# Kernel tuning notes

Measured on AMD Instinct MI355X. Metric: run time of the kernel, lower is better.

Reference implementation:

```python
import jax, jax.numpy as jnp
import numpy as np

B, H, W, C = 8, 256, 256, 180
HEADS, HEAD_DIM = 6, 30
WIN = (16, 16)
SPARSITY = 4


def setup_inputs() -> dict:
    key = jax.random.key(0)
    ks = jax.random.split(key, 6)
    bg = 1.0 / np.sqrt(3 * HEAD_DIM)          # ExpertGather init bound (1/sqrt(head_dim_out)) approx
    bs = 1.0 / np.sqrt(C * HEADS)             # ExpertScatter init bound
    return {
        "x": jax.random.normal(ks[0], (B, H, W, C), jnp.float32),
        "Wr": jax.random.normal(ks[1], (HEADS, C), jnp.float32) / np.sqrt(C),      # router Linear(dim, heads, bias=False)
        "Wqkv": jax.random.uniform(ks[2], (HEADS, C, 3 * HEAD_DIM), jnp.float32, -bg, bg),
        "Wo": jax.random.uniform(ks[3], (HEADS, HEAD_DIM, C), jnp.float32, -bs, bs),
        "Wp": jax.random.normal(ks[4], (C, C), jnp.float32) / np.sqrt(C),          # proj Linear(dim, dim)
        "bp": jnp.zeros((C,), jnp.float32),
    }


def reference(x, Wr, Wqkv, Wo, Wp, bp):
    wh, ww = WIN
    L = wh * ww  # tokens per window = 256
    # ---- window_partition: (B,H,W,C) -> (Bw, L, C)
    xw = x.reshape(B, H // wh, wh, W // ww, ww, C).transpose(0, 1, 3, 2, 4, 5).reshape(-1, L, C)
    Bw = xw.shape[0]
    # ---- router: sigmoid(Linear) -> (Bw, L, heads)
    logits = jax.nn.sigmoid(jnp.einsum('blc,ec->ble', xw, Wr))
    k = min(max(L // SPARSITY, 2), L)  # static: 64
    # ---- top-k including first token (get_topk_includefirst)
    tail = logits[:, 1:, :].transpose(0, 2, 1)          # (Bw, heads, L-1)
    tv, ti = jax.lax.top_k(tail, k - 1)                 # top k-1 over tokens 1..L-1
    ti = ti + 1
    fv = logits[:, 0, :][:, :, None]                    # (Bw, heads, 1)
    fi = jnp.zeros((Bw, HEADS, 1), jnp.int32)
    vals = jnp.concatenate([fv, tv], axis=2)            # (Bw, heads, k) sigmoid gates
    idx = jnp.concatenate([fi, ti], axis=2)             # (Bw, heads, k) token indices
    idx_flat = idx.reshape(Bw, HEADS * k)
    # ---- ExpertGather: per-head gather then per-head linear -> QKV
    Xg = jnp.take_along_axis(xw, idx_flat[:, :, None], axis=1).reshape(Bw, HEADS, k, C)
    qkv = jnp.einsum('beki,eij->bekj', Xg, Wqkv)        # (Bw, heads, k, 3*head_dim)
    Q, K, V = jnp.split(qkv, 3, axis=-1)
    # ---- scaled dot product attention over the k routed tokens per head
    scores = jnp.einsum('bekd,bejd->bekj', Q, K) / np.sqrt(HEAD_DIM).astype(np.float32)
    attn = jnp.einsum('bekj,bejd->bekd', jax.nn.softmax(scores, axis=-1), V)
    attn = attn * vals[..., None]                       # sigmoid gating
    # ---- ExpertScatter: per-head linear then scatter-add combine
    pre = jnp.einsum('bekj,eji->beki', attn, Wo)        # (Bw, heads, k, C)
    scattered = jnp.zeros((Bw, L, C), x.dtype).at[
        jnp.arange(Bw)[:, None], idx_flat
    ].add(pre.reshape(Bw, HEADS * k, C))
    # ---- window_reverse: (Bw, L, C) -> (B, H, W, C)
    y = scattered.reshape(B, H // wh, W // ww, wh, ww, C).transpose(0, 1, 3, 2, 4, 5).reshape(B, H, W, C)
    # ---- output projection (dropout prob = 0)
    return jnp.einsum('bhwc,oc->bhwo', y, Wp) + bp
```

## Files before the change

kernel.cpp:

```cpp
#include <hip/hip_runtime.h>
#include <math.h>

#define NB 8
#define NH 256
#define NW 256
#define NC 180
#define NE 6
#define HD 30
#define NL 256
#define NK 64
#define NWIN 2048

typedef __attribute__((ext_vector_type(8))) short bf16x8;
typedef __attribute__((ext_vector_type(4))) float f32x4;

union FU { bf16x8 f; unsigned u[4]; unsigned short s[8]; };

static __device__ __forceinline__ unsigned short f2bf(float x) {
    unsigned u = __float_as_uint(x);
    unsigned r = (u + 0x7FFFu + ((u >> 16) & 1u)) >> 16;
    return (unsigned short)r;
}
static __device__ __forceinline__ unsigned pk2(float a, float b) {
    return (unsigned)f2bf(a) | ((unsigned)f2bf(b) << 16);
}
static __device__ __forceinline__ bf16x8 ld8(const unsigned short* p) {
    FU t;
    *(uint2*)&t.u[0] = *(const uint2*)p;
    *(uint2*)&t.u[2] = *(const uint2*)(p + 16);
    return t.f;
}
static __device__ __forceinline__ bf16x8 ld16(const unsigned short* p) {
    FU t;
    *(uint4*)&t.u[0] = *(const uint4*)p;
    return t.f;
}
static __device__ __forceinline__ bf16x8 ld8q(const unsigned short* p) {
    FU t;
    t.u[0] = *(const unsigned*)p;
    t.u[1] = *(const unsigned*)(p + 2);
    t.u[2] = *(const unsigned*)(p + 16);
    t.u[3] = *(const unsigned*)(p + 18);
    return t.f;
}
static __device__ __forceinline__ bf16x8 pack8(float4 a, float4 b) {
    FU t;
    t.u[0] = pk2(a.x, a.y); t.u[1] = pk2(a.z, a.w);
    t.u[2] = pk2(b.x, b.y); t.u[3] = pk2(b.z, b.w);
    return t.f;
}

__global__ __launch_bounds__(256) void k_prep(
    const float* __restrict__ Wqkv, const float* __restrict__ Wo,
    const float* __restrict__ Wp,
    unsigned short* __restrict__ Wqkv_t, unsigned short* __restrict__ Wcomb_t)
{
    int i = blockIdx.x * 256 + threadIdx.x;
    if (i < NE * 96 * 192) {
        int q = i / 192, rem = i % 192;
        int h = q / 96, np = q % 96;
        int kt = rem / 32, lg = (rem % 32) / 8, e = rem % 8;
        int k = 32 * kt + 4 * lg + (e < 4 ? e : 12 + e);
        int sec = np >> 5, r = np & 31;
        float v = (r < 30 && k < NC) ? Wqkv[((long)h * NC + k) * 90 + sec * 30 + r] : 0.f;
        Wqkv_t[i] = f2bf(v);
    }
    if (i < NE * 192 * 32) {
        int q = i / 32, rem = i % 32;
        int h = q / 192, o = q % 192;
        int lg = rem / 8, e = rem % 8;
        int d = 4 * lg + (e < 4 ? e : 12 + e);
        float acc = 0.f;
        if (o < NC && d < HD) {
            const float* wo = Wo + ((long)h * HD + d) * NC;
            const float* wp = Wp + (long)o * NC;
            for (int c = 0; c < NC; ++c) acc += wo[c] * wp[c];
        }
        Wcomb_t[i] = f2bf(acc);
    }
}

__global__ __launch_bounds__(256) void k_router_topk(
    const float* __restrict__ x, const float* __restrict__ Wr,
    int* __restrict__ idx_g, float* __restrict__ vals_g)
{
    __shared__ float wr_s[NE * NC];
    __shared__ __align__(16) float xs[32 * 181];
    __shared__ float lg[NE * NL];

    const int w   = blockIdx.x;
    const int tid = threadIdx.x;
    const int b = w >> 8, hb = (w >> 4) & 15, wb = w & 15;
    const long win_base = (((long)b * NH + hb * 16) * NW + wb * 16) * NC;

    for (int f = tid; f < NE * NC; f += 256) wr_s[f] = Wr[f];
    __syncthreads();

    for (int tile = 0; tile < 8; ++tile) {
        for (int f = tid; f < 32 * NC; f += 256) {
            int tl = f / NC, ch = f % NC;
            int tok = tile * 32 + tl;
            int r = tok >> 4, cl = tok & 15;
            xs[tl * 181 + ch] = x[win_base + ((long)r * NW + cl) * NC + ch];
        }
        __syncthreads();
        if (tid < 192) {
            int tl = tid & 31, e = tid >> 5;
            float acc = 0.f;
            for (int c = 0; c < NC; ++c) acc += xs[tl * 181 + c] * wr_s[e * NC + c];
            lg[e * NL + tile * 32 + tl] = 1.0f / (1.0f + expf(-acc));
        }
        __syncthreads();
    }

    unsigned long long* keys = (unsigned long long*)xs;
    #pragma unroll
    for (int e = 0; e < NE; ++e) {
        unsigned kb = __float_as_uint(lg[e * NL + tid]);
        unsigned long long comp =
            ((unsigned long long)kb << 32) | (unsigned)(0xFFFFFFFFu - tid);
        if (tid == 0) comp = 0ull;
        keys[e * NL + tid] = comp;
    }
    __syncthreads();

    for (int k = 2; k <= 256; k <<= 1) {
        for (int j = k >> 1; j > 0; j >>= 1) {
            const int i = tid, ixj = i ^ j;
            if (ixj > i) {
                const bool up = ((i & k) == 0);
                #pragma unroll
                for (int e = 0; e < NE; ++e) {
                    unsigned long long a  = keys[e * NL + i];
                    unsigned long long bv = keys[e * NL + ixj];
                    bool sw = up ? (a < bv) : (a > bv);
                    if (sw) { keys[e * NL + i] = bv; keys[e * NL + ixj] = a; }
                }
            }
            __syncthreads();
        }
    }

    if (tid < NK - 1) {
        #pragma unroll
        for (int e = 0; e < NE; ++e) {
            unsigned long long kk = keys[e * NL + tid];
            int t = (int)(0xFFFFFFFFu - (unsigned)kk);
            idx_g[(w * NE + e) * NK + 1 + tid]  = t;
            vals_g[(w * NE + e) * NK + 1 + tid] = __uint_as_float((unsigned)(kk >> 32));
        }
    }
    if (tid == 0) {
        #pragma unroll
        for (int e = 0; e < NE; ++e) {
            idx_g[(w * NE + e) * NK]  = 0;
            vals_g[(w * NE + e) * NK] = lg[e * NL];
        }
    }
}

__global__ __launch_bounds__(256, 3) void k_attn(
    const float* __restrict__ x,
    const unsigned short* __restrict__ Wqkv_t,
    const int* __restrict__ idx_g, const float* __restrict__ vals_g,
    unsigned short* __restrict__ at_g)
{
    __shared__ char sm[34816];
    const int tid = threadIdx.x;
    const int wv = tid >> 6;
    const int ln = tid & 63;
    const int lr = ln & 15;
    const int lg = ln >> 4;

    const int bid = (blockIdx.x & 7) * 384 + (blockIdx.x >> 3);
    const int id = bid * 4 + wv;
    const int w = id / 6;
    const int h = id % 6;
    const int b = w >> 8, hb = (w >> 4) & 15, wb = w & 15;
    const long win_base = (((long)b * NH + hb * 16) * NW + wb * 16) * NC;

    unsigned short* q_s = (unsigned short*)(sm + wv * 8704);
    unsigned short* k_s = q_s + 2176;

    int tokr[4];
    #pragma unroll
    for (int t = 0; t < 4; ++t)
        tokr[t] = idx_g[((long)w * NE + h) * NK + 16 * t + lr];

    f32x4 acc[6][4];
    #pragma unroll
    for (int nt = 0; nt < 6; ++nt)
        #pragma unroll
        for (int mt = 0; mt < 4; ++mt) acc[nt][mt] = (f32x4){0.f, 0.f, 0.f, 0.f};

    const unsigned short* bb = Wqkv_t + ((long)h * 96 + lr) * 192 + 8 * lg;
    #pragma unroll
    for (int kt = 0; kt < 6; ++kt) {
        bf16x8 Amt[4];
        #pragma unroll
        for (int mt = 0; mt < 4; ++mt) {
            const float* xr = x + win_base +
                ((long)(tokr[mt] >> 4) * NW + (tokr[mt] & 15)) * NC;
            if (kt < 5) {
                float4 a  = *(const float4*)(xr + 4 * lg + 32 * kt);
                float4 b2 = *(const float4*)(xr + 4 * lg + 32 * kt + 16);
                Amt[mt] = pack8(a, b2);
            } else {
                float4 a  = *(const float4*)(xr + 4 * lg + 160);
                float4 b2 = make_float4(0.f, 0.f, 0.f, 0.f);
                if (lg == 0) b2 = *(const float4*)(xr + 176);
                Amt[mt] = pack8(a, b2);
            }
        }
        #pragma unroll
        for (int nt = 0; nt < 6; ++nt) {
            bf16x8 B = ld16(bb + nt * (16 * 192) + kt * 32);
            #pragma unroll
            for (int mt = 0; mt < 4; ++mt)
                acc[nt][mt] = __builtin_amdgcn_mfma_f32_16x16x32_bf16(Amt[mt], B, acc[nt][mt], 0, 0, 0);
        }
    }

    #pragma unroll
    for (int nt = 0; nt < 4; ++nt) {
        unsigned short* dst = (nt < 2 ? q_s : k_s) + 16 * (nt & 1) + lr;
        #pragma unroll
        for (int mt = 0; mt < 4; ++mt) {
            int row = 16 * mt + 4 * lg;
            dst[(row + 0) * 34] = f2bf(acc[nt][mt][0]);
            dst[(row + 1) * 34] = f2bf(acc[nt][mt][1]);
            dst[(row + 2) * 34] = f2bf(acc[nt][mt][2]);
            dst[(row + 3) * 34] = f2bf(acc[nt][mt][3]);
        }
    }
    unsigned V32[4][2][2];
    #pragma unroll
    for (int j = 0; j < 2; ++j)
        #pragma unroll
        for (int mt = 0; mt < 4; ++mt) {
            V32[mt][j][0] = pk2(acc[4 + j][mt][0], acc[4 + j][mt][1]);
            V32[mt][j][1] = pk2(acc[4 + j][mt][2], acc[4 + j][mt][3]);
        }

    __syncthreads();

    f32x4 s[4][4];
    {
        bf16x8 Bq[4];
        #pragma unroll
        for (int nt = 0; nt < 4; ++nt)
            Bq[nt] = ld8q(q_s + (16 * nt + lr) * 34 + 4 * lg);
        #pragma unroll
        for (int amt = 0; amt < 4; ++amt) {
            bf16x8 Ak = ld8q(k_s + (16 * amt + lr) * 34 + 4 * lg);
            #pragma unroll
            for (int nt = 0; nt < 4; ++nt)
                s[amt][nt] = __builtin_amdgcn_mfma_f32_16x16x32_bf16(
                    Ak, Bq[nt], (f32x4){0.f, 0.f, 0.f, 0.f}, 0, 0, 0);
        }
    }

    float gsc[4];
    #pragma unroll
    for (int nt = 0; nt < 4; ++nt) {
        float mx = -1e30f;
        #pragma unroll
        for (int amt = 0; amt < 4; ++amt)
            #pragma unroll
            for (int r = 0; r < 4; ++r) mx = fmaxf(mx, s[amt][nt][r]);
        mx = fmaxf(mx, __shfl_xor(mx, 16));
        mx = fmaxf(mx, __shfl_xor(mx, 32));
        float sum = 0.f;
        #pragma unroll
        for (int amt = 0; amt < 4; ++amt)
            #pragma unroll
            for (int r = 0; r < 4; ++r) {
                float p = __expf((s[amt][nt][r] - mx) * 0.18257418583505536f);
                s[amt][nt][r] = p;
                sum += p;
            }
        sum += __shfl_xor(sum, 16);
        sum += __shfl_xor(sum, 32);
        gsc[nt] = vals_g[((long)w * NE + h) * NK + 16 * nt + lr] / sum;
    }

    bf16x8 Av[2][2];
    #pragma unroll
    for (int amt = 0; amt < 2; ++amt)
        #pragma unroll
        for (int kt = 0; kt < 2; ++kt) {
            FU t;
            t.u[0] = V32[2 * kt][amt][0];
            t.u[1] = V32[2 * kt][amt][1];
            t.u[2] = V32[2 * kt + 1][amt][0];
            t.u[3] = V32[2 * kt + 1][amt][1];
            Av[amt][kt] = t.f;
        }
    #pragma unroll
    for (int nt = 0; nt < 4; ++nt) {
        bf16x8 Pb[2];
        float g = gsc[nt];
        #pragma unroll
        for (int kt = 0; kt < 2; ++kt) {
            FU t;
            t.u[0] = pk2(s[2 * kt][nt][0] * g, s[2 * kt][nt][1] * g);
            t.u[1] = pk2(s[2 * kt][nt][2] * g, s[2 * kt][nt][3] * g);
            t.u[2] = pk2(s[2 * kt + 1][nt][0] * g, s[2 * kt + 1][nt][1] * g);
            t.u[3] = pk2(s[2 * kt + 1][nt][2] * g, s[2 * kt + 1][nt][3] * g);
            Pb[kt] = t.f;
        }
        f32x4 a0 = (f32x4){0.f, 0.f, 0.f, 0.f};
        a0 = __builtin_amdgcn_mfma_f32_16x16x32_bf16(Av[0][0], Pb[0], a0, 0, 0, 0);
        a0 = __builtin_amdgcn_mfma_f32_16x16x32_bf16(Av[0][1], Pb[1], a0, 0, 0, 0);
        f32x4 a1 = (f32x4){0.f, 0.f, 0.f, 0.f};
        a1 = __builtin_amdgcn_mfma_f32_16x16x32_bf16(Av[1][0], Pb[0], a1, 0, 0, 0);
        a1 = __builtin_amdgcn_mfma_f32_16x16x32_bf16(Av[1][1], Pb[1], a1, 0, 0, 0);
        unsigned short* row = at_g + (((long)h * NWIN + w) * 64 + 16 * nt + lr) * 32 + 8 * lg;
        *(uint4*)row = make_uint4(pk2(a0[0], a0[1]), pk2(a0[2], a0[3]),
                                  pk2(a1[0], a1[1]), pk2(a1[2], a1[3]));
    }
}

__global__ __launch_bounds__(384, 2) void k_scatter(
    const unsigned short* __restrict__ at_g,
    const unsigned short* __restrict__ Wcomb_t,
    const float* __restrict__ bp,
    const int* __restrict__ idx_g,
    float* __restrict__ out)
{
    __shared__ float outf[256 * 49];
    __shared__ unsigned char idx_s[NE * NK];

    const int w = blockIdx.x;
    const int tid = threadIdx.x;
    const int b = w >> 8, hb = (w >> 4) & 15, wb = w & 15;

    const int wv = tid >> 6;
    const int ln = tid & 63;
    const int lr = ln & 15;
    const int lg = ln >> 4;

    idx_s[tid] = (unsigned char)idx_g[(long)w * NE * NK + tid];

    const int wcol = wv % 3;
    const int nth  = wv / 3;

    bf16x8 Bt[NE][2];
    #pragma unroll
    for (int h = 0; h < NE; ++h)
        #pragma unroll
        for (int t = 0; t < 2; ++t) {
            const int nt = 2 * nth + t;
            Bt[h][t] = ld16(at_g + (((long)h * NWIN + w) * 64 + 16 * nt + lr) * 32 + 8 * lg);
        }
    __syncthreads();

    int tokk[NE][2];
    #pragma unroll
    for (int h = 0; h < NE; ++h)
        #pragma unroll
        for (int t = 0; t < 2; ++t)
            tokk[h][t] = idx_s[h * NK + 16 * (2 * nth + t) + lr];

    #pragma unroll
    for (int p = 0; p < 4; ++p) {
        for (int f = tid; f < 256 * 49; f += 384) outf[f] = 0.f;
        __syncthreads();

        #pragma unroll
        for (int h = 0; h < NE; ++h) {
            bf16x8 Aw = ld16(Wcomb_t + ((long)h * 192 + p * 48 + 16 * wcol + lr) * 32 + 8 * lg);
            #pragma unroll
            for (int t = 0; t < 2; ++t) {
                f32x4 acc = __builtin_amdgcn_mfma_f32_16x16x32_bf16(
                    Aw, Bt[h][t], (f32x4){0.f, 0.f, 0.f, 0.f}, 0, 0, 0);
                float* dst = outf + tokk[h][t] * 49 + 16 * wcol + 4 * lg;
                dst[0] += acc[0];
                dst[1] += acc[1];
                dst[2] += acc[2];
                dst[3] += acc[3];
            }
            __syncthreads();
        }

        const int nf4 = (p == 3) ? 9 : 12;
        for (int f = tid; f < 256 * nf4; f += 384) {
            int t = f / nf4, j = f % nf4;
            int c = 48 * p + 4 * j;
            float4 o;
            o.x = outf[t * 49 + 4 * j]     + bp[c];
            o.y = outf[t * 49 + 4 * j + 1] + bp[c + 1];
            o.z = outf[t * 49 + 4 * j + 2] + bp[c + 2];
            o.w = outf[t * 49 + 4 * j + 3] + bp[c + 3];
            long obase = (((long)b * NH + hb * 16 + (t >> 4)) * NW + wb * 16 + (t & 15)) * NC + c;
            *(float4*)(out + obase) = o;
        }
        __syncthreads();
    }
}

extern "C" void kernel_launch(void* const* d_in, const int* in_sizes, int n_in,
                              void* d_out, int out_size, void* d_ws, size_t ws_size,
                              hipStream_t stream) {
    const float* x    = (const float*)d_in[0];
    const float* Wr   = (const float*)d_in[1];
    const float* Wqkv = (const float*)d_in[2];
    const float* Wo   = (const float*)d_in[3];
    const float* Wp   = (const float*)d_in[4];
    const float* bp   = (const float*)d_in[5];
    float* out = (float*)d_out;

    char* ws = (char*)d_ws;
    unsigned short* Wqkv_t  = (unsigned short*)ws;
    unsigned short* Wcomb_t = (unsigned short*)(ws + 221184);
    int*   idx_g  = (int*)(ws + 294912);
    float* vals_g = (float*)(ws + 294912 + (size_t)NWIN * NE * NK * 4);
    unsigned short* at_g = (unsigned short*)(ws + 294912 + 2 * (size_t)NWIN * NE * NK * 4);

    k_prep<<<432, 256, 0, stream>>>(Wqkv, Wo, Wp, Wqkv_t, Wcomb_t);
    k_router_topk<<<NWIN, 256, 0, stream>>>(x, Wr, idx_g, vals_g);
    k_attn<<<3072, 256, 0, stream>>>(x, Wqkv_t, idx_g, vals_g, at_g);
    k_scatter<<<NWIN, 384, 0, stream>>>(at_g, Wcomb_t, bp, idx_g, out);
}
```

Before: 569.4 us.

## Fuse attention and scatter kernels into one per-window block with LDS handoff

Merges k_attn and k_scatter into a single kernel in which each 384-thread block handles one window and each of its six waves computes one head. The attention output now stays in shared memory instead of going through a global bf16 buffer, and the routing indices are staged once in LDS. This removes a kernel launch and a global write/read round trip of the attention output. The cost is a larger shared-memory footprint per block (about 77 KB), which may reduce occupancy. The scatter phase also loses the register prefetch of its B operands and has to wait for all heads to finish first.

```diff
diff --git a/kernel.cpp b/kernel.cpp
--- a/kernel.cpp
+++ b/kernel.cpp
@@ -23,12 +23,6 @@
 }
 static __device__ __forceinline__ unsigned pk2(float a, float b) {
     return (unsigned)f2bf(a) | ((unsigned)f2bf(b) << 16);
-}
-static __device__ __forceinline__ bf16x8 ld8(const unsigned short* p) {
-    FU t;
-    *(uint2*)&t.u[0] = *(const uint2*)p;
-    *(uint2*)&t.u[2] = *(const uint2*)(p + 16);
-    return t.f;
 }
 static __device__ __forceinline__ bf16x8 ld16(const unsigned short* p) {
     FU t;
@@ -159,33 +153,39 @@
     }
 }
 
-__global__ __launch_bounds__(256, 3) void k_attn(
+__global__ __launch_bounds__(384, 3) void k_fused(
     const float* __restrict__ x,
     const unsigned short* __restrict__ Wqkv_t,
+    const unsigned short* __restrict__ Wcomb_t,
+    const float* __restrict__ bp,
     const int* __restrict__ idx_g, const float* __restrict__ vals_g,
-    unsigned short* __restrict__ at_g)
+    float* __restrict__ out)
 {
-    __shared__ char sm[34816];
+    __shared__ char smA[52224];
+    __shared__ unsigned short at_s[NE * 64 * 32];
+    __shared__ unsigned char idx_s[NE * NK];
+
+    const int w = blockIdx.x;
     const int tid = threadIdx.x;
+    const int b = w >> 8, hb = (w >> 4) & 15, wb = w & 15;
+    const long win_base = (((long)b * NH + hb * 16) * NW + wb * 16) * NC;
+
     const int wv = tid >> 6;
     const int ln = tid & 63;
     const int lr = ln & 15;
     const int lg = ln >> 4;
-
-    const int bid = (blockIdx.x & 7) * 384 + (blockIdx.x >> 3);
-    const int id = bid * 4 + wv;
-    const int w = id / 6;
-    const int h = id % 6;
-    const int b = w >> 8, hb = (w >> 4) & 15, wb = w & 15;
-    const long win_base = (((long)b * NH + hb * 16) * NW + wb * 16) * NC;
-
-    unsigned short* q_s = (unsigned short*)(sm + wv * 8704);
+    const int h = wv;
+
+    idx_s[tid] = (unsigned char)idx_g[(long)w * NE * NK + tid];
+    __syncthreads();
+
+    unsigned short* q_s = (unsigned short*)(smA + h * 8704);
     unsigned short* k_s = q_s + 2176;
 
     int tokr[4];
     #pragma unroll
     for (int t = 0; t < 4; ++t)
-        tokr[t] = idx_g[((long)w * NE + h) * NK + 16 * t + lr];
+        tokr[t] = idx_s[h * NK + 16 * t + lr];
 
     f32x4 acc[6][4];
     #pragma unroll
@@ -315,52 +315,15 @@
         f32x4 a1 = (f32x4){0.f, 0.f, 0.f, 0.f};
         a1 = __builtin_amdgcn_mfma_f32_16x16x32_bf16(Av[1][0], Pb[0], a1, 0, 0, 0);
         a1 = __builtin_amdgcn_mfma_f32_16x16x32_bf16(Av[1][1], Pb[1], a1, 0, 0, 0);
-        unsigned short* row = at_g + (((long)h * NWIN + w) * 64 + 16 * nt + lr) * 32 + 8 * lg;
+        unsigned short* row = at_s + ((h * 64 + 16 * nt + lr) * 32 + 8 * lg);
         *(uint4*)row = make_uint4(pk2(a0[0], a0[1]), pk2(a0[2], a0[3]),
                                   pk2(a1[0], a1[1]), pk2(a1[2], a1[3]));
     }
-}
-
-__global__ __launch_bounds__(384, 2) void k_scatter(
-    const unsigned short* __restrict__ at_g,
-    const unsigned short* __restrict__ Wcomb_t,
-    const float* __restrict__ bp,
-    const int* __restrict__ idx_g,
-    float* __restrict__ out)
-{
-    __shared__ float outf[256 * 49];
-    __shared__ unsigned char idx_s[NE * NK];
-
-    const int w = blockIdx.x;
-    const int tid = threadIdx.x;
-    const int b = w >> 8, hb = (w >> 4) & 15, wb = w & 15;
-
-    const int wv = tid >> 6;
-    const int ln = tid & 63;
-    const int lr = ln & 15;
-    const int lg = ln >> 4;
-
-    idx_s[tid] = (unsigned char)idx_g[(long)w * NE * NK + tid];
-
+    __syncthreads();
+
+    float* outf = (float*)smA;
     const int wcol = wv % 3;
     const int nth  = wv / 3;
-
-    bf16x8 Bt[NE][2];
-    #pragma unroll
-    for (int h = 0; h < NE; ++h)
-        #pragma unroll
-        for (int t = 0; t < 2; ++t) {
-            const int nt = 2 * nth + t;
-            Bt[h][t] = ld16(at_g + (((long)h * NWIN + w) * 64 + 16 * nt + lr) * 32 + 8 * lg);
-        }
-    __syncthreads();
-
-    int tokk[NE][2];
-    #pragma unroll
-    for (int h = 0; h < NE; ++h)
-        #pragma unroll
-        for (int t = 0; t < 2; ++t)
-            tokk[h][t] = idx_s[h * NK + 16 * (2 * nth + t) + lr];
 
     #pragma unroll
     for (int p = 0; p < 4; ++p) {
@@ -368,17 +331,20 @@
         __syncthreads();
 
         #pragma unroll
-        for (int h = 0; h < NE; ++h) {
-            bf16x8 Aw = ld16(Wcomb_t + ((long)h * 192 + p * 48 + 16 * wcol + lr) * 32 + 8 * lg);
+        for (int hh = 0; hh < NE; ++hh) {
+            bf16x8 Aw = ld16(Wcomb_t + ((long)hh * 192 + p * 48 + 16 * wcol + lr) * 32 + 8 * lg);
             #pragma unroll
             for (int t = 0; t < 2; ++t) {
-                f32x4 acc = __builtin_amdgcn_mfma_f32_16x16x32_bf16(
-                    Aw, Bt[h][t], (f32x4){0.f, 0.f, 0.f, 0.f}, 0, 0, 0);
-                float* dst = outf + tokk[h][t] * 49 + 16 * wcol + 4 * lg;
-                dst[0] += acc[0];
-                dst[1] += acc[1];
-                dst[2] += acc[2];
-                dst[3] += acc[3];
+                const int nt = 2 * nth + t;
+                bf16x8 Bt = ld16(at_s + ((hh * 64 + 16 * nt + lr) * 32 + 8 * lg));
+                f32x4 pacc = __builtin_amdgcn_mfma_f32_16x16x32_bf16(
+                    Aw, Bt, (f32x4){0.f, 0.f, 0.f, 0.f}, 0, 0, 0);
+                int tok = idx_s[hh * NK + 16 * nt + lr];
+                float* dst = outf + tok * 49 + 16 * wcol + 4 * lg;
+                dst[0] += pacc[0];
+                dst[1] += pacc[1];
+                dst[2] += pacc[2];
+                dst[3] += pacc[3];
             }
             __syncthreads();
         }
@@ -415,10 +381,9 @@
     unsigned short* Wcomb_t = (unsigned short*)(ws + 221184);
     int*   idx_g  = (int*)(ws + 294912);
     float* vals_g = (float*)(ws + 294912 + (size_t)NWIN * NE * NK * 4);
-    unsigned short* at_g = (unsigned short*)(ws + 294912 + 2 * (size_t)NWIN * NE * NK * 4);
 
     k_prep<<<432, 256, 0, stream>>>(Wqkv, Wo, Wp, Wqkv_t, Wcomb_t);
     k_router_topk<<<NWIN, 256, 0, stream>>>(x, Wr, idx_g, vals_g);
-    k_attn<<<3072, 256, 0, stream>>>(x, Wqkv_t, idx_g, vals_g, at_g);
-    k_scatter<<<NWIN, 384, 0, stream>>>(at_g, Wcomb_t, bp, idx_g, out);
-}
+    k_fused<<<NWIN, 384, 0, stream>>>(x, Wqkv_t, Wcomb_t, bp,
+                                      idx_g, vals_g, out);
+}
```

Measured after the change: 700.3 us. +23.0%, slower.
